# Kernel optimization log

Measured on AMD Instinct MI355X. Metric: run time of the kernel, lower is better.

## Reference

```python
import jax, jax.numpy as jnp
import numpy as np

N, K, C = 200000, 27, 64


def setup_inputs() -> dict:
    key = jax.random.key(0)
    k1, k2, k3, k4 = jax.random.split(key, 4)
    data = jax.random.normal(k1, (N, C), dtype=jnp.float32)
    # Xavier-like scale for depthwise weights (kdim, 1, C)
    weights = jax.random.normal(k2, (K, 1, C), dtype=jnp.float32) * 0.1
    neigh = jax.random.randint(k3, (N, K), 0, N, dtype=jnp.int32)
    invalid = jax.random.uniform(k4, (N, K)) < 0.05
    neigh = jnp.where(invalid, -1, neigh)
    return {"data": data, "weights": weights, "neigh": neigh}


def reference(data, weights, neigh):
    # buffer[i,k,c] = data[neigh[i,k], c] if neigh[i,k] >= 0 else 0
    valid = neigh >= 0                                   # [N, K]
    gathered = jnp.where(valid[:, :, None],
                         data[jnp.clip(neigh, 0)],       # [N, K, C]
                         jnp.zeros((), dtype=data.dtype))
    w = weights.reshape(K, C)                            # flatten(0,1)
    out = jnp.einsum('ikc,kc->ic', gathered, w)          # depthwise conv
    return out
```

## Files before the change

kernel.cpp:

```cpp
#include <hip/hip_runtime.h>
#include <stdint.h>


typedef float    v4f __attribute__((ext_vector_type(4)));
typedef uint32_t v2u __attribute__((ext_vector_type(2)));

constexpr int K   = 27;
constexpr int C   = 64;
constexpr int RPB = 32;

__global__ __launch_bounds__(256) void convert_kernel(
    const v4f* __restrict__ in,
    uint32_t*  __restrict__ outq,
    float*     __restrict__ scales,
    int nrows)
{
    const int l16 = threadIdx.x & 15;
    const int grp = threadIdx.x >> 4;
    const int r   = blockIdx.x * 16 + grp;
    if (r >= nrows) return;

    v4f a = __builtin_nontemporal_load(in + r * 16 + l16);
    float m = fmaxf(fmaxf(fabsf(a.x), fabsf(a.y)),
                    fmaxf(fabsf(a.z), fabsf(a.w)));
    m = fmaxf(m, __shfl_xor(m, 1));
    m = fmaxf(m, __shfl_xor(m, 2));
    m = fmaxf(m, __shfl_xor(m, 4));
    m = fmaxf(m, __shfl_xor(m, 8));

    const float inv = (m > 0.f) ? 127.f / m : 0.f;
    const int q0 = __float2int_rn(a.x * inv);
    const int q1 = __float2int_rn(a.y * inv);
    const int q2 = __float2int_rn(a.z * inv);
    const int q3 = __float2int_rn(a.w * inv);
    outq[r * 16 + l16] = (uint32_t)(q0 & 255)
                       | ((uint32_t)(q1 & 255) << 8)
                       | ((uint32_t)(q2 & 255) << 16)
                       | ((uint32_t)q3 << 24);
    if (l16 == 0) scales[r] = m * (1.f / 127.f);
}

__global__ __launch_bounds__(256) void gather_kernel(
    const v2u*   __restrict__ dataq,
    const float* __restrict__ scales,
    const float* __restrict__ weights,
    const int*   __restrict__ neigh,
    v4f*         __restrict__ out4,
    int nrows)
{
    __shared__ float w_lds[K * C];
    __shared__ int   n_lds[RPB * K];

    const int tid = threadIdx.x;
    for (int idx = tid; idx < K * C / 4; idx += 256)
        ((v4f*)w_lds)[idx] = ((const v4f*)weights)[idx];

    const long nbase = (long)blockIdx.x * RPB * K;
    const long ntot  = (long)nrows * K;
    for (int idx = tid; idx < RPB * K; idx += 256) {
        const long g = nbase + idx;
        n_lds[idx] = (g < ntot) ? __builtin_nontemporal_load(neigh + g) : -1;
    }
    __syncthreads();

    const int l     = tid & 7;
    const int group = tid >> 3;
    const int row   = blockIdx.x * RPB + group;
    if (row >= nrows) return;

    const int* __restrict__ nrow = n_lds + group * K;

    v4f acc0 = (v4f){0.f, 0.f, 0.f, 0.f};
    v4f acc1 = (v4f){0.f, 0.f, 0.f, 0.f};

    #pragma unroll
    for (int b = 0; b < K; b += 9) {
        int   nk[9];
        v2u   d[9];
        float s[9];
        #pragma unroll
        for (int j = 0; j < 9; ++j) nk[j] = nrow[b + j];
        #pragma unroll
        for (int j = 0; j < 9; ++j) {
            const int n  = nk[j];
            const int nz = (n < 0) ? 0 : n;
            d[j] = dataq[nz * 8 + l];
            const float sv = scales[nz];
            s[j] = (n < 0) ? 0.f : sv;
        }
        #pragma unroll
        for (int j = 0; j < 9; ++j) {
            const int k = b + j;
            const v4f* wv = (const v4f*)(w_lds + k * C + l * 8);
            const v4f ws0 = wv[0] * s[j];
            const v4f ws1 = wv[1] * s[j];
            const uint32_t lo = d[j].x, hi = d[j].y;
            acc0.x += (float)(int8_t)(lo      ) * ws0.x;
            acc0.y += (float)(int8_t)(lo >>  8) * ws0.y;
            acc0.z += (float)(int8_t)(lo >> 16) * ws0.z;
            acc0.w += (float)((int)lo >> 24)    * ws0.w;
            acc1.x += (float)(int8_t)(hi      ) * ws1.x;
            acc1.y += (float)(int8_t)(hi >>  8) * ws1.y;
            acc1.z += (float)(int8_t)(hi >> 16) * ws1.z;
            acc1.w += (float)((int)hi >> 24)    * ws1.w;
        }
    }

    v4f* o = out4 + row * (C / 4) + l * 2;
    __builtin_nontemporal_store(acc0, o);
    __builtin_nontemporal_store(acc1, o + 1);
}

extern "C" void kernel_launch(void* const* d_in, const int* in_sizes, int n_in,
                              void* d_out, int out_size, void* d_ws, size_t ws_size,
                              hipStream_t stream) {
    const float* data    = (const float*)d_in[0];
    const float* weights = (const float*)d_in[1];
    const int*   neigh   = (const int*)d_in[2];
    v4f*         out4    = (v4f*)d_out;

    const int nrows = in_sizes[0] / C;
    uint32_t* dataq8 = (uint32_t*)d_ws;
    float*    scales = (float*)((char*)d_ws + (size_t)nrows * 64);

    convert_kernel<<<(nrows + 15) / 16, 256, 0, stream>>>(
        (const v4f*)data, dataq8, scales, nrows);

    const int blocks = (nrows + RPB - 1) / RPB;
    gather_kernel<<<blocks, 256, 0, stream>>>(
        (const v2u*)dataq8, scales, weights, neigh, out4, nrows);
}
```

Before: 198.7 us.

## Fuse quantize and gather into one persistent kernel with a grid barrier

Merges the int8 conversion pass and the gather-conv pass into a single persistent kernel with a fixed grid of 695 blocks. The blocks sync through an atomic-counter grid barrier that is reset by a memset before launch. Invalid neighbours are redirected to an extra zero row with zero scale, which removes the per-load branch and select. Each block now processes 9 row groups, so the barrier and LDS weight load are amortised. The intent is to remove a kernel launch and its tail gap. The barrier can deadlock if the 695 blocks cannot all be resident at once, and it adds a memset plus spin-wait cost.

```diff
diff --git a/kernel.cpp b/kernel.cpp
--- a/kernel.cpp
+++ b/kernel.cpp
@@ -5,110 +5,130 @@
 typedef float    v4f __attribute__((ext_vector_type(4)));
 typedef uint32_t v2u __attribute__((ext_vector_type(2)));
 
-constexpr int K   = 27;
-constexpr int C   = 64;
-constexpr int RPB = 32;
+constexpr int K    = 27;
+constexpr int C    = 64;
+constexpr int RPB  = 32;
+constexpr int G    = 9;
+constexpr int GRID = 695;
+constexpr int ROWS_PER_BLK = G * RPB;
+constexpr int NPB  = ROWS_PER_BLK * K;
 
-__global__ __launch_bounds__(256) void convert_kernel(
-    const v4f* __restrict__ in,
-    uint32_t*  __restrict__ outq,
-    float*     __restrict__ scales,
-    int nrows)
-{
-    const int l16 = threadIdx.x & 15;
-    const int grp = threadIdx.x >> 4;
-    const int r   = blockIdx.x * 16 + grp;
-    if (r >= nrows) return;
-
-    v4f a = __builtin_nontemporal_load(in + r * 16 + l16);
-    float m = fmaxf(fmaxf(fabsf(a.x), fabsf(a.y)),
-                    fmaxf(fabsf(a.z), fabsf(a.w)));
-    m = fmaxf(m, __shfl_xor(m, 1));
-    m = fmaxf(m, __shfl_xor(m, 2));
-    m = fmaxf(m, __shfl_xor(m, 4));
-    m = fmaxf(m, __shfl_xor(m, 8));
-
-    const float inv = (m > 0.f) ? 127.f / m : 0.f;
-    const int q0 = __float2int_rn(a.x * inv);
-    const int q1 = __float2int_rn(a.y * inv);
-    const int q2 = __float2int_rn(a.z * inv);
-    const int q3 = __float2int_rn(a.w * inv);
-    outq[r * 16 + l16] = (uint32_t)(q0 & 255)
-                       | ((uint32_t)(q1 & 255) << 8)
-                       | ((uint32_t)(q2 & 255) << 16)
-                       | ((uint32_t)q3 << 24);
-    if (l16 == 0) scales[r] = m * (1.f / 127.f);
-}
-
-__global__ __launch_bounds__(256) void gather_kernel(
-    const v2u*   __restrict__ dataq,
-    const float* __restrict__ scales,
+__global__ __launch_bounds__(256, 4) void fused_kernel(
+    const v4f*   __restrict__ in,
+    uint32_t*    __restrict__ dataq,
+    float*       __restrict__ scales,
     const float* __restrict__ weights,
     const int*   __restrict__ neigh,
     v4f*         __restrict__ out4,
+    unsigned*    __restrict__ bar_ctr,
     int nrows)
 {
+    const int tid = threadIdx.x;
+
+    {
+        const int total  = (nrows + 1) * 16;
+        const int stride = GRID * 256;
+        for (int t = blockIdx.x * 256 + tid; t < total; t += stride) {
+            const int r = t >> 4;
+            if (r >= nrows) {
+                dataq[t] = 0u;
+                if ((t & 15) == 0) scales[r] = 0.f;
+                continue;
+            }
+            v4f a = __builtin_nontemporal_load(in + t);
+            float m = fmaxf(fmaxf(fabsf(a.x), fabsf(a.y)),
+                            fmaxf(fabsf(a.z), fabsf(a.w)));
+            m = fmaxf(m, __shfl_xor(m, 1));
+            m = fmaxf(m, __shfl_xor(m, 2));
+            m = fmaxf(m, __shfl_xor(m, 4));
+            m = fmaxf(m, __shfl_xor(m, 8));
+            const float inv = (m > 0.f) ? 127.f / m : 0.f;
+            const int q0 = __float2int_rn(a.x * inv);
+            const int q1 = __float2int_rn(a.y * inv);
+            const int q2 = __float2int_rn(a.z * inv);
+            const int q3 = __float2int_rn(a.w * inv);
+            dataq[t] = (uint32_t)(q0 & 255)
+                     | ((uint32_t)(q1 & 255) << 8)
+                     | ((uint32_t)(q2 & 255) << 16)
+                     | ((uint32_t)q3 << 24);
+            if ((t & 15) == 0) scales[r] = m * (1.f / 127.f);
+        }
+    }
+
+    __syncthreads();
+    if (tid == 0) {
+        __threadfence();
+        atomicAdd(bar_ctr, 1u);
+        while (__hip_atomic_load(bar_ctr, __ATOMIC_ACQUIRE,
+                                 __HIP_MEMORY_SCOPE_AGENT) < (unsigned)GRID)
+            __builtin_amdgcn_s_sleep(8);
+        __threadfence();
+    }
+    __syncthreads();
+
     __shared__ float w_lds[K * C];
-    __shared__ int   n_lds[RPB * K];
+    __shared__ int   n_lds[NPB];
 
-    const int tid = threadIdx.x;
     for (int idx = tid; idx < K * C / 4; idx += 256)
         ((v4f*)w_lds)[idx] = ((const v4f*)weights)[idx];
 
-    const long nbase = (long)blockIdx.x * RPB * K;
+    const long nbase = (long)blockIdx.x * NPB;
     const long ntot  = (long)nrows * K;
-    for (int idx = tid; idx < RPB * K; idx += 256) {
-        const long g = nbase + idx;
-        n_lds[idx] = (g < ntot) ? __builtin_nontemporal_load(neigh + g) : -1;
+    for (int idx = tid; idx < NPB; idx += 256) {
+        const long p = nbase + idx;
+        const int v = (p < ntot) ? __builtin_nontemporal_load(neigh + p) : -1;
+        n_lds[idx] = (v < 0) ? nrows : v;
     }
     __syncthreads();
 
     const int l     = tid & 7;
     const int group = tid >> 3;
-    const int row   = blockIdx.x * RPB + group;
-    if (row >= nrows) return;
-
-    const int* __restrict__ nrow = n_lds + group * K;
-
-    v4f acc0 = (v4f){0.f, 0.f, 0.f, 0.f};
-    v4f acc1 = (v4f){0.f, 0.f, 0.f, 0.f};
+    const v2u* __restrict__ dq2 = (const v2u*)dataq;
 
     #pragma unroll
-    for (int b = 0; b < K; b += 9) {
-        int   nk[9];
-        v2u   d[9];
-        float s[9];
+    for (int g = 0; g < G; ++g) {
+        const int row = blockIdx.x * ROWS_PER_BLK + g * RPB + group;
+        const int* __restrict__ nrow = n_lds + (g * RPB + group) * K;
+
+        v4f acc0 = (v4f){0.f, 0.f, 0.f, 0.f};
+        v4f acc1 = (v4f){0.f, 0.f, 0.f, 0.f};
+
         #pragma unroll
-        for (int j = 0; j < 9; ++j) nk[j] = nrow[b + j];
-        #pragma unroll
-        for (int j = 0; j < 9; ++j) {
-            const int n  = nk[j];
-            const int nz = (n < 0) ? 0 : n;
-            d[j] = dataq[nz * 8 + l];
-            const float sv = scales[nz];
-            s[j] = (n < 0) ? 0.f : sv;
+        for (int b = 0; b < K; b += 9) {
+            int   nk[9];
+            v2u   d[9];
+            float s[9];
+            #pragma unroll
+            for (int j = 0; j < 9; ++j) nk[j] = nrow[b + j];
+            #pragma unroll
+            for (int j = 0; j < 9; ++j) {
+                d[j] = dq2[nk[j] * 8 + l];
+                s[j] = scales[nk[j]];
+            }
+            #pragma unroll
+            for (int j = 0; j < 9; ++j) {
+                const int k = b + j;
+                const v4f* wv = (const v4f*)(w_lds + k * C + l * 8);
+                const v4f ws0 = wv[0] * s[j];
+                const v4f ws1 = wv[1] * s[j];
+                const uint32_t lo = d[j].x, hi = d[j].y;
+                acc0.x += (float)(int8_t)(lo      ) * ws0.x;
+                acc0.y += (float)(int8_t)(lo >>  8) * ws0.y;
+                acc0.z += (float)(int8_t)(lo >> 16) * ws0.z;
+                acc0.w += (float)((int)lo >> 24)    * ws0.w;
+                acc1.x += (float)(int8_t)(hi      ) * ws1.x;
+                acc1.y += (float)(int8_t)(hi >>  8) * ws1.y;
+                acc1.z += (float)(int8_t)(hi >> 16) * ws1.z;
+                acc1.w += (float)((int)hi >> 24)    * ws1.w;
+            }
         }
-        #pragma unroll
-        for (int j = 0; j < 9; ++j) {
-            const int k = b + j;
-            const v4f* wv = (const v4f*)(w_lds + k * C + l * 8);
-            const v4f ws0 = wv[0] * s[j];
-            const v4f ws1 = wv[1] * s[j];
-            const uint32_t lo = d[j].x, hi = d[j].y;
-            acc0.x += (float)(int8_t)(lo      ) * ws0.x;
-            acc0.y += (float)(int8_t)(lo >>  8) * ws0.y;
-            acc0.z += (float)(int8_t)(lo >> 16) * ws0.z;
-            acc0.w += (float)((int)lo >> 24)    * ws0.w;
-            acc1.x += (float)(int8_t)(hi      ) * ws1.x;
-            acc1.y += (float)(int8_t)(hi >>  8) * ws1.y;
-            acc1.z += (float)(int8_t)(hi >> 16) * ws1.z;
-            acc1.w += (float)((int)hi >> 24)    * ws1.w;
+
+        if (row < nrows) {
+            v4f* o = out4 + row * (C / 4) + l * 2;
+            __builtin_nontemporal_store(acc0, o);
+            __builtin_nontemporal_store(acc1, o + 1);
         }
     }
-
-    v4f* o = out4 + row * (C / 4) + l * 2;
-    __builtin_nontemporal_store(acc0, o);
-    __builtin_nontemporal_store(acc1, o + 1);
 }
 
 extern "C" void kernel_launch(void* const* d_in, const int* in_sizes, int n_in,
@@ -120,13 +140,17 @@
     v4f*         out4    = (v4f*)d_out;
 
     const int nrows = in_sizes[0] / C;
-    uint32_t* dataq8 = (uint32_t*)d_ws;
-    float*    scales = (float*)((char*)d_ws + (size_t)nrows * 64);
 
-    convert_kernel<<<(nrows + 15) / 16, 256, 0, stream>>>(
-        (const v4f*)data, dataq8, scales, nrows);
+    uint32_t* dataq = (uint32_t*)d_ws;
+    const size_t dq_bytes = (size_t)(nrows + 1) * 64;
+    float* scales = (float*)((char*)d_ws + dq_bytes);
+    const size_t sc_bytes = (size_t)(nrows + 1) * 4;
+    unsigned* bar_ctr = (unsigned*)((char*)d_ws +
+        ((dq_bytes + sc_bytes + 127) & ~(size_t)127));
 
-    const int blocks = (nrows + RPB - 1) / RPB;
-    gather_kernel<<<blocks, 256, 0, stream>>>(
-        (const v2u*)dataq8, scales, weights, neigh, out4, nrows);
+    hipMemsetAsync(bar_ctr, 0, 128, stream);
+
+    fused_kernel<<<GRID, 256, 0, stream>>>(
+        (const v4f*)data, dataq, scales, weights, neigh, out4,
+        bar_ctr, nrows);
 }
```

Result: slower. 586.5 us (+195.2%).
